# Kernel optimization log

Measured on AMD Instinct MI355X. Metric: run time of the kernel, lower is better.

## Reference

```python
import jax, jax.numpy as jnp
import numpy as np

N = 50000      # nodes
E = 800000     # edges (avg degree 16)
F_IN = 128     # num_node_features
D = 64         # embedding_size (= per-head out_channels)
H = 4          # heads
ED = 20        # edge_dim (hardcoded in module)
SLOPE = 0.2    # GATv2 leaky_relu negative slope
N_LAYERS = 3   # conv applied 3 times with shared weights


def setup_inputs() -> dict:
    key = jax.random.key(0)
    ks = jax.random.split(key, 12)
    s = 0.1
    return {
        "x": jax.random.normal(ks[0], (N, F_IN), jnp.float32),
        "edge_attr": jax.random.normal(ks[1], (E, 2), jnp.float32),
        "edge_index": jax.random.randint(ks[2], (2, E), 0, N, dtype=jnp.int32),
        # f: Linear(F_IN, D)
        "f_W": jax.random.normal(ks[3], (F_IN, D), jnp.float32) * s,
        "f_b": jnp.zeros((D,), jnp.float32),
        # fe: Linear(2, ED)
        "fe_W": jax.random.normal(ks[4], (2, ED), jnp.float32) * s,
        "fe_b": jnp.zeros((ED,), jnp.float32),
        # GATv2Conv lin_l / lin_r: Linear(D, H*D)
        "Wl": jax.random.normal(ks[5], (D, H * D), jnp.float32) * s,
        "bl": jnp.zeros((H * D,), jnp.float32),
        "Wr": jax.random.normal(ks[6], (D, H * D), jnp.float32) * s,
        "br": jnp.zeros((H * D,), jnp.float32),
        # lin_edge: Linear(ED, H*D, bias=False)
        "We": jax.random.normal(ks[7], (ED, H * D), jnp.float32) * s,
        # attention vector att: [H, D]
        "att": jax.random.normal(ks[8], (H, D), jnp.float32) * s,
        # final bias (concat=False -> size D)
        "bias": jnp.zeros((D,), jnp.float32),
    }


def _gatv2_conv(h, e_emb, src, dst, Wl, bl, Wr, br, We, att, bias):
    # h: [N, D], e_emb: [E, ED], src/dst: [E]
    xl = (h @ Wl + bl).reshape(-1, H, D)        # source transform  [N,H,D]
    xr = (h @ Wr + br).reshape(-1, H, D)        # target transform  [N,H,D]
    ee = (e_emb @ We).reshape(-1, H, D)         # edge transform    [E,H,D]
    m = jax.nn.leaky_relu(xl[src] + xr[dst] + ee, SLOPE)  # [E,H,D]
    score = jnp.einsum('ehd,hd->eh', m, att)    # [E,H]
    # segment softmax over incoming edges of each dst node
    smax = jax.ops.segment_max(score, dst, num_segments=N)   # [N,H]
    ex = jnp.exp(score - smax[dst])
    denom = jax.ops.segment_sum(ex, dst, num_segments=N)     # [N,H]
    alpha = ex / denom[dst]                                  # [E,H]
    out = jax.ops.segment_sum(alpha[:, :, None] * xl[src], dst, num_segments=N)  # [N,H,D]
    return out.mean(axis=1) + bias              # concat=False -> head mean, [N,D]


def reference(x, edge_attr, edge_index, f_W, f_b, fe_W, fe_b, Wl, bl, Wr, br, We, att, bias):
    src, dst = edge_index[0], edge_index[1]
    h = jax.nn.relu(x @ f_W + f_b)
    e = jax.nn.relu(edge_attr @ fe_W + fe_b)
    for _ in range(N_LAYERS):
        h = jax.nn.relu(_gatv2_conv(h, e, src, dst, Wl, bl, Wr, br, We, att, bias))
    return h
```

## Files before the change

kernel.cpp:

```cpp
#include <hip/hip_runtime.h>
#include <math.h>

typedef float v2f __attribute__((ext_vector_type(2)));

#define LN2_INV 1.4426950408889634f

__device__ __forceinline__ float fexp2(float x) {
#if __has_builtin(__builtin_amdgcn_exp2f)
    return __builtin_amdgcn_exp2f(x);
#else
    return exp2f(x);
#endif
}

__device__ __forceinline__ v2f pk_fma(v2f a, v2f b, v2f c) {
    asm("v_pk_fma_f32 %0, %1, %2, %0" : "+v"(c) : "v"(a), "v"(b));
    return c;
}
__device__ __forceinline__ v2f pk_fma_s(v2f a_s, v2f b, v2f c) {
    asm("v_pk_fma_f32 %0, %1, %2, %0" : "+v"(c) : "s"(a_s), "v"(b));
    return c;
}
__device__ __forceinline__ v2f pk_mul_s(v2f a_s, v2f b) {
    v2f d;
    asm("v_pk_mul_f32 %0, %1, %2" : "=v"(d) : "s"(a_s), "v"(b));
    return d;
}

#define DPP_ROW_ADD(V, CTRL) \
    V += __int_as_float(__builtin_amdgcn_update_dpp(0, __float_as_int(V), CTRL, 0xf, 0xf, true));

__global__ __launch_bounds__(256) void k_h0(const float* __restrict__ x,
                                            const float* __restrict__ fW,
                                            const float* __restrict__ fb,
                                            float* __restrict__ h0) {
    __shared__ __align__(16) float xs[8 * 128];
    int t = threadIdx.x;
    int base = blockIdx.x * 8;
#pragma unroll
    for (int r = 0; r < 4; ++r) { int j = r * 256 + t; xs[j] = x[base * 128 + j]; }
    __syncthreads();
    int c = t & 63, half = t >> 6;
    float acc0 = fb[c], acc1 = fb[c];
    int m0 = half, m1 = half + 4;
#pragma unroll 8
    for (int k0 = 0; k0 < 128; k0 += 4) {
        float4 a = *(const float4*)&xs[m0 * 128 + k0];
        float4 b = *(const float4*)&xs[m1 * 128 + k0];
        float w0 = fW[(k0 + 0) * 64 + c], w1 = fW[(k0 + 1) * 64 + c];
        float w2 = fW[(k0 + 2) * 64 + c], w3 = fW[(k0 + 3) * 64 + c];
        acc0 = fmaf(a.x, w0, fmaf(a.y, w1, fmaf(a.z, w2, fmaf(a.w, w3, acc0))));
        acc1 = fmaf(b.x, w0, fmaf(b.y, w1, fmaf(b.z, w2, fmaf(b.w, w3, acc1))));
    }
    h0[(base + m0) * 64 + c] = fmaxf(acc0, 0.f);
    h0[(base + m1) * 64 + c] = fmaxf(acc1, 0.f);
}

__global__ __launch_bounds__(256) void k_xlxr(const float* __restrict__ h,
                                              const float* __restrict__ Wl,
                                              const float* __restrict__ Wr,
                                              const float* __restrict__ bl,
                                              const float* __restrict__ br,
                                              float* __restrict__ xl,
                                              float* __restrict__ xr) {
    __shared__ __align__(16) float hs[16 * 64];
    int t = threadIdx.x;
    int base = blockIdx.x * 16;
#pragma unroll
    for (int r = 0; r < 4; ++r) hs[r * 256 + t] = h[base * 64 + r * 256 + t];
    __syncthreads();
    float bL = bl[t], bR = br[t];
    float accl[16], accr[16];
#pragma unroll
    for (int m = 0; m < 16; ++m) { accl[m] = bL; accr[m] = bR; }
#pragma unroll 4
    for (int k0 = 0; k0 < 64; k0 += 4) {
        float wl[4], wr[4];
#pragma unroll
        for (int q = 0; q < 4; ++q) {
            wl[q] = Wl[(k0 + q) * 256 + t];
            wr[q] = Wr[(k0 + q) * 256 + t];
        }
#pragma unroll
        for (int m = 0; m < 16; ++m) {
            float4 hv = *(const float4*)&hs[m * 64 + k0];
            accl[m] = fmaf(hv.x, wl[0], fmaf(hv.y, wl[1], fmaf(hv.z, wl[2], fmaf(hv.w, wl[3], accl[m]))));
            accr[m] = fmaf(hv.x, wr[0], fmaf(hv.y, wr[1], fmaf(hv.z, wr[2], fmaf(hv.w, wr[3], accr[m]))));
        }
    }
#pragma unroll
    for (int m = 0; m < 16; ++m) {
        xl[(base + m) * 256 + t] = accl[m];
        xr[(base + m) * 256 + t] = accr[m];
    }
}

__global__ void k_zero(int* __restrict__ deg, int* __restrict__ counter,
                       int* __restrict__ rec, int Nn, int Ee) {
    int i = blockIdx.x * 256 + threadIdx.x;
    if (i < Nn) deg[i] = 0;
    if (i == 0) *counter = 0;
    if (blockIdx.x == 0 && threadIdx.x < 96) rec[(size_t)Ee * 24 + threadIdx.x] = 0;
}

__global__ void k_count(const int* __restrict__ dstArr, int* __restrict__ deg, int Ee) {
    int e = blockIdx.x * 256 + threadIdx.x;
    if (e < Ee) atomicAdd(&deg[dstArr[e]], 1);
}

__global__ void k_alloc(const int* __restrict__ deg, int* __restrict__ counter,
                        int* __restrict__ start, int* __restrict__ cursor, int Nn) {
    int n = blockIdx.x * 256 + threadIdx.x;
    if (n < Nn) {
        int d = deg[n];
        int b = atomicAdd(counter, d);
        start[n] = b;
        cursor[n] = b;
    }
}

__global__ void k_fill(const int* __restrict__ dstArr, const int* __restrict__ srcArr,
                       const float* __restrict__ eattr, const float* __restrict__ feW,
                       const float* __restrict__ feb, int* __restrict__ cursor,
                       int* __restrict__ rec, int Ee) {
    int e = blockIdx.x * 256 + threadIdx.x;
    if (e >= Ee) return;
    float a0 = eattr[2 * e], a1 = eattr[2 * e + 1];
    int p = atomicAdd(&cursor[dstArr[e]], 1);
    float* r = (float*)(rec + (size_t)p * 24);
    float s[20];
#pragma unroll
    for (int k = 0; k < 20; ++k)
        s[k] = fmaxf(fmaf(a0, feW[k], fmaf(a1, feW[20 + k], feb[k])), 0.f);
#pragma unroll
    for (int j = 0; j < 5; ++j)
        ((float4*)r)[j] = make_float4(s[4 * j], s[4 * j + 1], s[4 * j + 2], s[4 * j + 3]);
    ((int*)r)[20] = srcArr[e];
}

#define LOAD_BLOCK(SK, E_) do {                                              \
    const float* _rp = rf + (size_t)(E_) * 24;                               \
    _Pragma("unroll")                                                        \
    for (int _k = 0; _k < 20; ++_k) SK[_k] = _rp[_k];                        \
} while (0)

#define COMPUTE_EDGE(SK, XL) do {                                            \
    v2f _sp0 = {SK[0], SK[1]};                                               \
    v2f _a0 = pk_mul_s(_sp0, weI0[0]);                                       \
    v2f _a1 = pk_mul_s(_sp0, weI1[0]);                                       \
    v2f _a2 = pk_mul_s(_sp0, weI2[0]);                                       \
    v2f _a3 = pk_mul_s(_sp0, weI3[0]);                                       \
    _Pragma("unroll")                                                        \
    for (int _p = 1; _p < 10; ++_p) {                                        \
        v2f _s = {SK[2 * _p], SK[2 * _p + 1]};                               \
        _a0 = pk_fma_s(_s, weI0[_p], _a0);                                   \
        _a1 = pk_fma_s(_s, weI1[_p], _a1);                                   \
        _a2 = pk_fma_s(_s, weI2[_p], _a2);                                   \
        _a3 = pk_fma_s(_s, weI3[_p], _a3);                                   \
    }                                                                        \
    float _v0 = (XL.x + xrv.x) + (_a0.x + _a0.y);                            \
    float _v1 = (XL.y + xrv.y) + (_a1.x + _a1.y);                            \
    float _v2 = (XL.z + xrv.z) + (_a2.x + _a2.y);                            \
    float _v3 = (XL.w + xrv.w) + (_a3.x + _a3.y);                            \
    float _m0 = fmaxf(_v0, 0.2f * _v0);                                      \
    float _m1 = fmaxf(_v1, 0.2f * _v1);                                      \
    float _m2 = fmaxf(_v2, 0.2f * _v2);                                      \
    float _m3 = fmaxf(_v3, 0.2f * _v3);                                      \
    float _ps = fmaf(at0, _m0, fmaf(at1, _m1, fmaf(at2, _m2, at3 * _m3)));   \
    DPP_ROW_ADD(_ps, 0x111)                                                  \
    DPP_ROW_ADD(_ps, 0x112)                                                  \
    DPP_ROW_ADD(_ps, 0x114)                                                  \
    DPP_ROW_ADD(_ps, 0x118)                                                  \
    float _sc = __int_as_float(                                              \
        __builtin_amdgcn_ds_bpermute(bperm, __float_as_int(_ps)));           \
    float _w = fexp2(_sc);                                                   \
    l += _w;                                                                 \
    v2f _w2 = {_w, _w};                                                      \
    v2f _xl01 = {XL.x, XL.y}, _xl23 = {XL.z, XL.w};                          \
    acc01 = pk_fma(_w2, _xl01, acc01);                                       \
    acc23 = pk_fma(_w2, _xl23, acc23);                                       \
} while (0)

__global__ __launch_bounds__(256, 3) void k_edge(
    const float4* __restrict__ xl4p, const float4* __restrict__ xr4p,
    const float* __restrict__ att, const float4* __restrict__ We4,
    const int* __restrict__ rec, const int* __restrict__ start,
    const int* __restrict__ deg, const float* __restrict__ bias,
    float* __restrict__ hout, int Nn) {
    const int lane = threadIdx.x & 63;
    const int n = (int)((blockIdx.x * 256u + threadIdx.x) >> 6);
    if (n >= Nn) return;

    const int dn = __builtin_amdgcn_readfirstlane(deg[n]);
    float4 bias4 = ((const float4*)bias)[lane & 15];
    if (dn == 0) {
        if (lane < 16) {
            float4 o = make_float4(fmaxf(bias4.x, 0.f), fmaxf(bias4.y, 0.f),
                                   fmaxf(bias4.z, 0.f), fmaxf(bias4.w, 0.f));
            ((float4*)hout)[(size_t)n * 16 + lane] = o;
        }
        return;
    }
    const int s0 = __builtin_amdgcn_readfirstlane(start[n]);
    const float* rf = (const float*)rec + (size_t)s0 * 24;
    const int* ri = rec + (size_t)s0 * 24;

    float4 attv = ((const float4*)att)[lane];
    float at0 = attv.x * LN2_INV, at1 = attv.y * LN2_INV;
    float at2 = attv.z * LN2_INV, at3 = attv.w * LN2_INV;
    float4 xrv = xr4p[(size_t)n * 64 + lane];
    v2f weI0[10], weI1[10], weI2[10], weI3[10];
#pragma unroll
    for (int p = 0; p < 10; ++p) {
        float4 w0 = We4[(2 * p) * 64 + lane];
        float4 w1 = We4[(2 * p + 1) * 64 + lane];
        weI0[p].x = w0.x; weI0[p].y = w1.x;
        weI1[p].x = w0.y; weI1[p].y = w1.y;
        weI2[p].x = w0.z; weI2[p].y = w1.z;
        weI3[p].x = w0.w; weI3[p].y = w1.w;
    }
    const int bperm = ((lane & 48) | 15) << 2;

    v2f acc01 = {0.f, 0.f}, acc23 = {0.f, 0.f};
    float l = 0.f;

    float skA[20], skB[20];
    LOAD_BLOCK(skA, 0);
    LOAD_BLOCK(skB, 1);
    int sA0 = ri[20];
    int sB0 = ri[44];
    float4 xlA = xl4p[(size_t)(unsigned)sA0 * 64 + lane];
    float4 xlB = xl4p[(size_t)(unsigned)sB0 * 64 + lane];
    int srcA = ri[2 * 24 + 20];
    int srcB = ri[3 * 24 + 20];

    const int nfull = dn >> 1;
    for (int t = 0; t < nfull; ++t) {
        float4 xlA2 = xl4p[(size_t)(unsigned)srcA * 64 + lane];
        srcA = ri[(size_t)(2 * t + 4) * 24 + 20];
        COMPUTE_EDGE(skA, xlA);
        LOAD_BLOCK(skA, 2 * t + 2);
        xlA = xlA2;
        float4 xlB2 = xl4p[(size_t)(unsigned)srcB * 64 + lane];
        srcB = ri[(size_t)(2 * t + 5) * 24 + 20];
        COMPUTE_EDGE(skB, xlB);
        LOAD_BLOCK(skB, 2 * t + 3);
        xlB = xlB2;
    }
    if (dn & 1) COMPUTE_EDGE(skA, xlA);

    float inv = 0.25f / l;
    float4 r = make_float4(acc01.x * inv, acc01.y * inv, acc23.x * inv, acc23.y * inv);
    r.x += __shfl_xor(r.x, 16, 64); r.x += __shfl_xor(r.x, 32, 64);
    r.y += __shfl_xor(r.y, 16, 64); r.y += __shfl_xor(r.y, 32, 64);
    r.z += __shfl_xor(r.z, 16, 64); r.z += __shfl_xor(r.z, 32, 64);
    r.w += __shfl_xor(r.w, 16, 64); r.w += __shfl_xor(r.w, 32, 64);
    if (lane < 16) {
        float4 o = make_float4(fmaxf(r.x + bias4.x, 0.f), fmaxf(r.y + bias4.y, 0.f),
                               fmaxf(r.z + bias4.z, 0.f), fmaxf(r.w + bias4.w, 0.f));
        ((float4*)hout)[(size_t)n * 16 + lane] = o;
    }
}

extern "C" void kernel_launch(void* const* d_in, const int* in_sizes, int n_in,
                              void* d_out, int out_size, void* d_ws, size_t ws_size,
                              hipStream_t stream) {
    const float* x     = (const float*)d_in[0];
    const float* eattr = (const float*)d_in[1];
    const int*   eidx  = (const int*)d_in[2];
    const float* fW    = (const float*)d_in[3];
    const float* fb    = (const float*)d_in[4];
    const float* feW   = (const float*)d_in[5];
    const float* feb   = (const float*)d_in[6];
    const float* Wl    = (const float*)d_in[7];
    const float* bl    = (const float*)d_in[8];
    const float* Wr    = (const float*)d_in[9];
    const float* br    = (const float*)d_in[10];
    const float* We    = (const float*)d_in[11];
    const float* att   = (const float*)d_in[12];
    const float* bias  = (const float*)d_in[13];
    float* out = (float*)d_out;

    const int N = in_sizes[0] / 128;
    const int E = in_sizes[1] / 2;
    const int* srcArr = eidx;
    const int* dstArr = eidx + E;

    char* p = (char*)d_ws;
    auto alloc = [&](size_t bytes) -> char* {
        char* r = p;
        p += (bytes + 255) & ~(size_t)255;
        return r;
    };
    float* hA   = (float*)alloc((size_t)N * 64 * 4);
    float* hB   = (float*)alloc((size_t)N * 64 * 4);
    float* xl   = (float*)alloc((size_t)N * 256 * 4);
    float* xr   = (float*)alloc((size_t)N * 256 * 4);
    int* deg    = (int*)alloc((size_t)N * 4);
    int* start  = (int*)alloc((size_t)N * 4);
    int* cursor = (int*)alloc((size_t)N * 4);
    int* counter = (int*)alloc(256);
    int* rec    = (int*)alloc((size_t)(E + 4) * 24 * 4);

    k_h0<<<N / 8, 256, 0, stream>>>(x, fW, fb, hA);
    k_zero<<<(N + 255) / 256, 256, 0, stream>>>(deg, counter, rec, N, E);
    k_count<<<(E + 255) / 256, 256, 0, stream>>>(dstArr, deg, E);
    k_alloc<<<(N + 255) / 256, 256, 0, stream>>>(deg, counter, start, cursor, N);
    k_fill<<<(E + 255) / 256, 256, 0, stream>>>(dstArr, srcArr, eattr, feW, feb,
                                                cursor, rec, E);

    const float* hin = hA;
    for (int layer = 0; layer < 3; ++layer) {
        float* hout = (layer == 2) ? out : ((layer == 0) ? hB : hA);
        k_xlxr<<<N / 16, 256, 0, stream>>>(hin, Wl, Wr, bl, br, xl, xr);
        k_edge<<<(N * 64) / 256, 256, 0, stream>>>(
            (const float4*)xl, (const float4*)xr, att, (const float4*)We,
            rec, start, deg, bias, hout, N);
        hin = hout;
    }
}
```

Measured before the change: 967.2 us.

## Split edge source indices into separate array and deepen xl gather prefetch

```diff
diff --git a/kernel.cpp b/kernel.cpp
--- a/kernel.cpp
+++ b/kernel.cpp
@@ -2,6 +2,7 @@
 #include <math.h>
 
 typedef float v2f __attribute__((ext_vector_type(2)));
+typedef float v4f __attribute__((ext_vector_type(4)));
 
 #define LN2_INV 1.4426950408889634f
 
@@ -26,6 +27,9 @@
     asm("v_pk_mul_f32 %0, %1, %2" : "=v"(d) : "s"(a_s), "v"(b));
     return d;
 }
+
+#define PIN_V(X) asm("" : "+v"(X))
+#define PIN_S(X) asm("" : "+s"(X))
 
 #define DPP_ROW_ADD(V, CTRL) \
     V += __int_as_float(__builtin_amdgcn_update_dpp(0, __float_as_int(V), CTRL, 0xf, 0xf, true));
@@ -96,11 +100,13 @@
 }
 
 __global__ void k_zero(int* __restrict__ deg, int* __restrict__ counter,
-                       int* __restrict__ rec, int Nn, int Ee) {
+                       int* __restrict__ rec, int* __restrict__ sidx,
+                       int Nn, int Ee) {
     int i = blockIdx.x * 256 + threadIdx.x;
     if (i < Nn) deg[i] = 0;
     if (i == 0) *counter = 0;
-    if (blockIdx.x == 0 && threadIdx.x < 96) rec[(size_t)Ee * 24 + threadIdx.x] = 0;
+    if (blockIdx.x == 0 && threadIdx.x < 160) rec[(size_t)Ee * 20 + threadIdx.x] = 0;
+    if (blockIdx.x == 0 && threadIdx.x < 8) sidx[Ee + threadIdx.x] = 0;
 }
 
 __global__ void k_count(const int* __restrict__ dstArr, int* __restrict__ deg, int Ee) {
@@ -122,12 +128,12 @@
 __global__ void k_fill(const int* __restrict__ dstArr, const int* __restrict__ srcArr,
                        const float* __restrict__ eattr, const float* __restrict__ feW,
                        const float* __restrict__ feb, int* __restrict__ cursor,
-                       int* __restrict__ rec, int Ee) {
+                       int* __restrict__ rec, int* __restrict__ sidx, int Ee) {
     int e = blockIdx.x * 256 + threadIdx.x;
     if (e >= Ee) return;
     float a0 = eattr[2 * e], a1 = eattr[2 * e + 1];
     int p = atomicAdd(&cursor[dstArr[e]], 1);
-    float* r = (float*)(rec + (size_t)p * 24);
+    float* r = (float*)(rec + (size_t)p * 20);
     float s[20];
 #pragma unroll
     for (int k = 0; k < 20; ++k)
@@ -135,11 +141,11 @@
 #pragma unroll
     for (int j = 0; j < 5; ++j)
         ((float4*)r)[j] = make_float4(s[4 * j], s[4 * j + 1], s[4 * j + 2], s[4 * j + 3]);
-    ((int*)r)[20] = srcArr[e];
+    sidx[p] = srcArr[e];
 }
 
 #define LOAD_BLOCK(SK, E_) do {                                              \
-    const float* _rp = rf + (size_t)(E_) * 24;                               \
+    const float* _rp = rf + (size_t)(E_) * 20;                               \
     _Pragma("unroll")                                                        \
     for (int _k = 0; _k < 20; ++_k) SK[_k] = _rp[_k];                        \
 } while (0)
@@ -182,33 +188,33 @@
 } while (0)
 
 __global__ __launch_bounds__(256, 3) void k_edge(
-    const float4* __restrict__ xl4p, const float4* __restrict__ xr4p,
+    const v4f* __restrict__ xl4p, const v4f* __restrict__ xr4p,
     const float* __restrict__ att, const float4* __restrict__ We4,
-    const int* __restrict__ rec, const int* __restrict__ start,
-    const int* __restrict__ deg, const float* __restrict__ bias,
-    float* __restrict__ hout, int Nn) {
+    const int* __restrict__ rec, const int* __restrict__ sidx,
+    const int* __restrict__ start, const int* __restrict__ deg,
+    const float* __restrict__ bias, float* __restrict__ hout, int Nn) {
     const int lane = threadIdx.x & 63;
     const int n = (int)((blockIdx.x * 256u + threadIdx.x) >> 6);
     if (n >= Nn) return;
 
     const int dn = __builtin_amdgcn_readfirstlane(deg[n]);
-    float4 bias4 = ((const float4*)bias)[lane & 15];
+    v4f bias4 = ((const v4f*)bias)[lane & 15];
     if (dn == 0) {
         if (lane < 16) {
-            float4 o = make_float4(fmaxf(bias4.x, 0.f), fmaxf(bias4.y, 0.f),
-                                   fmaxf(bias4.z, 0.f), fmaxf(bias4.w, 0.f));
-            ((float4*)hout)[(size_t)n * 16 + lane] = o;
+            v4f o = {fmaxf(bias4.x, 0.f), fmaxf(bias4.y, 0.f),
+                     fmaxf(bias4.z, 0.f), fmaxf(bias4.w, 0.f)};
+            ((v4f*)hout)[(size_t)n * 16 + lane] = o;
         }
         return;
     }
     const int s0 = __builtin_amdgcn_readfirstlane(start[n]);
-    const float* rf = (const float*)rec + (size_t)s0 * 24;
-    const int* ri = rec + (size_t)s0 * 24;
+    const float* rf = (const float*)rec + (size_t)s0 * 20;
+    const int* sI = sidx + s0;
 
     float4 attv = ((const float4*)att)[lane];
     float at0 = attv.x * LN2_INV, at1 = attv.y * LN2_INV;
     float at2 = attv.z * LN2_INV, at3 = attv.w * LN2_INV;
-    float4 xrv = xr4p[(size_t)n * 64 + lane];
+    v4f xrv = xr4p[(size_t)n * 64 + lane];
     v2f weI0[10], weI1[10], weI2[10], weI3[10];
 #pragma unroll
     for (int p = 0; p < 10; ++p) {
@@ -227,38 +233,43 @@
     float skA[20], skB[20];
     LOAD_BLOCK(skA, 0);
     LOAD_BLOCK(skB, 1);
-    int sA0 = ri[20];
-    int sB0 = ri[44];
-    float4 xlA = xl4p[(size_t)(unsigned)sA0 * 64 + lane];
-    float4 xlB = xl4p[(size_t)(unsigned)sB0 * 64 + lane];
-    int srcA = ri[2 * 24 + 20];
-    int srcB = ri[3 * 24 + 20];
+    int e0 = sI[0], e1 = sI[1], e2 = sI[2], e3 = sI[3];
+    int srcA = sI[4], srcB = sI[5];
+    v4f xlA  = xl4p[(size_t)(unsigned)e0 * 64 + lane];
+    v4f xlB  = xl4p[(size_t)(unsigned)e1 * 64 + lane];
+    v4f xlA1 = xl4p[(size_t)(unsigned)e2 * 64 + lane];
+    v4f xlB1 = xl4p[(size_t)(unsigned)e3 * 64 + lane];
 
     const int nfull = dn >> 1;
+#pragma unroll 2
     for (int t = 0; t < nfull; ++t) {
-        float4 xlA2 = xl4p[(size_t)(unsigned)srcA * 64 + lane];
-        srcA = ri[(size_t)(2 * t + 4) * 24 + 20];
+        v4f xlA2 = xl4p[(size_t)(unsigned)srcA * 64 + lane];
+        PIN_V(xlA2);
+        srcA = sI[2 * t + 6];
+        PIN_S(srcA);
         COMPUTE_EDGE(skA, xlA);
         LOAD_BLOCK(skA, 2 * t + 2);
-        xlA = xlA2;
-        float4 xlB2 = xl4p[(size_t)(unsigned)srcB * 64 + lane];
-        srcB = ri[(size_t)(2 * t + 5) * 24 + 20];
+        xlA = xlA1; xlA1 = xlA2;
+        v4f xlB2 = xl4p[(size_t)(unsigned)srcB * 64 + lane];
+        PIN_V(xlB2);
+        srcB = sI[2 * t + 7];
+        PIN_S(srcB);
         COMPUTE_EDGE(skB, xlB);
         LOAD_BLOCK(skB, 2 * t + 3);
-        xlB = xlB2;
+        xlB = xlB1; xlB1 = xlB2;
     }
     if (dn & 1) COMPUTE_EDGE(skA, xlA);
 
     float inv = 0.25f / l;
-    float4 r = make_float4(acc01.x * inv, acc01.y * inv, acc23.x * inv, acc23.y * inv);
+    v4f r = {acc01.x * inv, acc01.y * inv, acc23.x * inv, acc23.y * inv};
     r.x += __shfl_xor(r.x, 16, 64); r.x += __shfl_xor(r.x, 32, 64);
     r.y += __shfl_xor(r.y, 16, 64); r.y += __shfl_xor(r.y, 32, 64);
     r.z += __shfl_xor(r.z, 16, 64); r.z += __shfl_xor(r.z, 32, 64);
     r.w += __shfl_xor(r.w, 16, 64); r.w += __shfl_xor(r.w, 32, 64);
     if (lane < 16) {
-        float4 o = make_float4(fmaxf(r.x + bias4.x, 0.f), fmaxf(r.y + bias4.y, 0.f),
-                               fmaxf(r.z + bias4.z, 0.f), fmaxf(r.w + bias4.w, 0.f));
-        ((float4*)hout)[(size_t)n * 16 + lane] = o;
+        v4f o = {fmaxf(r.x + bias4.x, 0.f), fmaxf(r.y + bias4.y, 0.f),
+                 fmaxf(r.z + bias4.z, 0.f), fmaxf(r.w + bias4.w, 0.f)};
+        ((v4f*)hout)[(size_t)n * 16 + lane] = o;
     }
 }
 
@@ -300,22 +311,23 @@
     int* start  = (int*)alloc((size_t)N * 4);
     int* cursor = (int*)alloc((size_t)N * 4);
     int* counter = (int*)alloc(256);
-    int* rec    = (int*)alloc((size_t)(E + 4) * 24 * 4);
+    int* rec    = (int*)alloc((size_t)(E + 8) * 20 * 4);
+    int* sidx   = (int*)alloc((size_t)(E + 8) * 4);
 
     k_h0<<<N / 8, 256, 0, stream>>>(x, fW, fb, hA);
-    k_zero<<<(N + 255) / 256, 256, 0, stream>>>(deg, counter, rec, N, E);
+    k_zero<<<(N + 255) / 256, 256, 0, stream>>>(deg, counter, rec, sidx, N, E);
     k_count<<<(E + 255) / 256, 256, 0, stream>>>(dstArr, deg, E);
     k_alloc<<<(N + 255) / 256, 256, 0, stream>>>(deg, counter, start, cursor, N);
     k_fill<<<(E + 255) / 256, 256, 0, stream>>>(dstArr, srcArr, eattr, feW, feb,
-                                                cursor, rec, E);
+                                                cursor, rec, sidx, E);
 
     const float* hin = hA;
     for (int layer = 0; layer < 3; ++layer) {
         float* hout = (layer == 2) ? out : ((layer == 0) ? hB : hA);
         k_xlxr<<<N / 16, 256, 0, stream>>>(hin, Wl, Wr, bl, br, xl, xr);
         k_edge<<<(N * 64) / 256, 256, 0, stream>>>(
-            (const float4*)xl, (const float4*)xr, att, (const float4*)We,
-            rec, start, deg, bias, hout, N);
+            (const v4f*)xl, (const v4f*)xr, att, (const float4*)We,
+            rec, sidx, start, deg, bias, hout, N);
         hin = hout;
     }
 }
```

Measured after the change: 953.6 us. Within noise of the previous version (-1.4%).

## Prefetch edge sources via readlane, deepen xl prefetch, vectorize record loads

Applied to the files above, without the earlier changes.

```diff
diff --git a/kernel.cpp b/kernel.cpp
--- a/kernel.cpp
+++ b/kernel.cpp
@@ -13,21 +13,21 @@
 #endif
 }
 
+__device__ __forceinline__ int rdlane_i(int v, int k) {
+    return __builtin_amdgcn_readlane(v, k);
+}
+
 __device__ __forceinline__ v2f pk_fma(v2f a, v2f b, v2f c) {
     asm("v_pk_fma_f32 %0, %1, %2, %0" : "+v"(c) : "v"(a), "v"(b));
     return c;
 }
-__device__ __forceinline__ v2f pk_fma_s(v2f a_s, v2f b, v2f c) {
-    asm("v_pk_fma_f32 %0, %1, %2, %0" : "+v"(c) : "s"(a_s), "v"(b));
-    return c;
-}
-__device__ __forceinline__ v2f pk_mul_s(v2f a_s, v2f b) {
+__device__ __forceinline__ v2f pk_mul(v2f a, v2f b) {
     v2f d;
-    asm("v_pk_mul_f32 %0, %1, %2" : "=v"(d) : "s"(a_s), "v"(b));
+    asm("v_pk_mul_f32 %0, %1, %2" : "=v"(d) : "v"(a), "v"(b));
     return d;
 }
 
-#define DPP_ROW_ADD(V, CTRL) \
+#define DPP_ADD(V, CTRL) \
     V += __int_as_float(__builtin_amdgcn_update_dpp(0, __float_as_int(V), CTRL, 0xf, 0xf, true));
 
 __global__ __launch_bounds__(256) void k_h0(const float* __restrict__ x,
@@ -138,25 +138,30 @@
     ((int*)r)[20] = srcArr[e];
 }
 
-#define LOAD_BLOCK(SK, E_) do {                                              \
-    const float* _rp = rf + (size_t)(E_) * 24;                               \
-    _Pragma("unroll")                                                        \
-    for (int _k = 0; _k < 20; ++_k) SK[_k] = _rp[_k];                        \
+#define VLOAD_REC(SK4, E_) do {                                              \
+    const float4* _rp = (const float4*)(rf + (size_t)(E_) * 24);             \
+    SK4[0] = _rp[0]; SK4[1] = _rp[1]; SK4[2] = _rp[2];                       \
+    SK4[3] = _rp[3]; SK4[4] = _rp[4];                                        \
 } while (0)
 
-#define COMPUTE_EDGE(SK, XL) do {                                            \
-    v2f _sp0 = {SK[0], SK[1]};                                               \
-    v2f _a0 = pk_mul_s(_sp0, weI0[0]);                                       \
-    v2f _a1 = pk_mul_s(_sp0, weI1[0]);                                       \
-    v2f _a2 = pk_mul_s(_sp0, weI2[0]);                                       \
-    v2f _a3 = pk_mul_s(_sp0, weI3[0]);                                       \
+#define COMPUTE_EDGE(SK4, XL) do {                                           \
+    v2f _a0, _a1, _a2, _a3;                                                  \
+    {                                                                        \
+        v2f _sp = {SK4[0].x, SK4[0].y};                                      \
+        _a0 = pk_mul(_sp, weI0[0]);                                          \
+        _a1 = pk_mul(_sp, weI1[0]);                                          \
+        _a2 = pk_mul(_sp, weI2[0]);                                          \
+        _a3 = pk_mul(_sp, weI3[0]);                                          \
+    }                                                                        \
     _Pragma("unroll")                                                        \
     for (int _p = 1; _p < 10; ++_p) {                                        \
-        v2f _s = {SK[2 * _p], SK[2 * _p + 1]};                               \
-        _a0 = pk_fma_s(_s, weI0[_p], _a0);                                   \
-        _a1 = pk_fma_s(_s, weI1[_p], _a1);                                   \
-        _a2 = pk_fma_s(_s, weI2[_p], _a2);                                   \
-        _a3 = pk_fma_s(_s, weI3[_p], _a3);                                   \
+        int _j = _p >> 1;                                                    \
+        v2f _sp = (_p & 1) ? (v2f){SK4[_j].z, SK4[_j].w}                     \
+                           : (v2f){SK4[_j].x, SK4[_j].y};                    \
+        _a0 = pk_fma(_sp, weI0[_p], _a0);                                    \
+        _a1 = pk_fma(_sp, weI1[_p], _a1);                                    \
+        _a2 = pk_fma(_sp, weI2[_p], _a2);                                    \
+        _a3 = pk_fma(_sp, weI3[_p], _a3);                                    \
     }                                                                        \
     float _v0 = (XL.x + xrv.x) + (_a0.x + _a0.y);                            \
     float _v1 = (XL.y + xrv.y) + (_a1.x + _a1.y);                            \
@@ -167,13 +172,11 @@
     float _m2 = fmaxf(_v2, 0.2f * _v2);                                      \
     float _m3 = fmaxf(_v3, 0.2f * _v3);                                      \
     float _ps = fmaf(at0, _m0, fmaf(at1, _m1, fmaf(at2, _m2, at3 * _m3)));   \
-    DPP_ROW_ADD(_ps, 0x111)                                                  \
-    DPP_ROW_ADD(_ps, 0x112)                                                  \
-    DPP_ROW_ADD(_ps, 0x114)                                                  \
-    DPP_ROW_ADD(_ps, 0x118)                                                  \
-    float _sc = __int_as_float(                                              \
-        __builtin_amdgcn_ds_bpermute(bperm, __float_as_int(_ps)));           \
-    float _w = fexp2(_sc);                                                   \
+    DPP_ADD(_ps, 0x121)                                                      \
+    DPP_ADD(_ps, 0x122)                                                      \
+    DPP_ADD(_ps, 0x124)                                                      \
+    DPP_ADD(_ps, 0x128)                                                      \
+    float _w = fexp2(_ps);                                                   \
     l += _w;                                                                 \
     v2f _w2 = {_w, _w};                                                      \
     v2f _xl01 = {XL.x, XL.y}, _xl23 = {XL.z, XL.w};                          \
@@ -192,11 +195,11 @@
     if (n >= Nn) return;
 
     const int dn = __builtin_amdgcn_readfirstlane(deg[n]);
-    float4 bias4 = ((const float4*)bias)[lane & 15];
     if (dn == 0) {
         if (lane < 16) {
-            float4 o = make_float4(fmaxf(bias4.x, 0.f), fmaxf(bias4.y, 0.f),
-                                   fmaxf(bias4.z, 0.f), fmaxf(bias4.w, 0.f));
+            float4 b4 = ((const float4*)bias)[lane];
+            float4 o = make_float4(fmaxf(b4.x, 0.f), fmaxf(b4.y, 0.f),
+                                   fmaxf(b4.z, 0.f), fmaxf(b4.w, 0.f));
             ((float4*)hout)[(size_t)n * 16 + lane] = o;
         }
         return;
@@ -204,6 +207,9 @@
     const int s0 = __builtin_amdgcn_readfirstlane(start[n]);
     const float* rf = (const float*)rec + (size_t)s0 * 24;
     const int* ri = rec + (size_t)s0 * 24;
+
+    const int lc = (lane < dn) ? lane : (dn - 1);
+    int srcv = rec[(size_t)(s0 + lc) * 24 + 20];
 
     float4 attv = ((const float4*)att)[lane];
     float at0 = attv.x * LN2_INV, at1 = attv.y * LN2_INV;
@@ -219,35 +225,40 @@
         weI2[p].x = w0.z; weI2[p].y = w1.z;
         weI3[p].x = w0.w; weI3[p].y = w1.w;
     }
-    const int bperm = ((lane & 48) | 15) << 2;
 
     v2f acc01 = {0.f, 0.f}, acc23 = {0.f, 0.f};
     float l = 0.f;
 
-    float skA[20], skB[20];
-    LOAD_BLOCK(skA, 0);
-    LOAD_BLOCK(skB, 1);
-    int sA0 = ri[20];
-    int sB0 = ri[44];
-    float4 xlA = xl4p[(size_t)(unsigned)sA0 * 64 + lane];
-    float4 xlB = xl4p[(size_t)(unsigned)sB0 * 64 + lane];
-    int srcA = ri[2 * 24 + 20];
-    int srcB = ri[3 * 24 + 20];
+    auto get_src = [&](int j) -> int {
+        return (j < 64) ? rdlane_i(srcv, j) : ri[(size_t)j * 24 + 20];
+    };
+
+    float4 skA4[5], skB4[5];
+    VLOAD_REC(skA4, 0);
+    VLOAD_REC(skB4, 1);
+    int j1 = (1 < dn) ? 1 : (dn - 1);
+    int j2 = (2 < dn) ? 2 : (dn - 1);
+    int j3 = (3 < dn) ? 3 : (dn - 1);
+    float4 xlA  = xl4p[(size_t)(unsigned)get_src(0) * 64 + lane];
+    float4 xlB  = xl4p[(size_t)(unsigned)get_src(j1) * 64 + lane];
+    float4 xlA1 = xl4p[(size_t)(unsigned)get_src(j2) * 64 + lane];
+    float4 xlB1 = xl4p[(size_t)(unsigned)get_src(j3) * 64 + lane];
 
     const int nfull = dn >> 1;
     for (int t = 0; t < nfull; ++t) {
-        float4 xlA2 = xl4p[(size_t)(unsigned)srcA * 64 + lane];
-        srcA = ri[(size_t)(2 * t + 4) * 24 + 20];
-        COMPUTE_EDGE(skA, xlA);
-        LOAD_BLOCK(skA, 2 * t + 2);
-        xlA = xlA2;
-        float4 xlB2 = xl4p[(size_t)(unsigned)srcB * 64 + lane];
-        srcB = ri[(size_t)(2 * t + 5) * 24 + 20];
-        COMPUTE_EDGE(skB, xlB);
-        LOAD_BLOCK(skB, 2 * t + 3);
-        xlB = xlB2;
-    }
-    if (dn & 1) COMPUTE_EDGE(skA, xlA);
+        int i = 2 * t;
+        int jA = (i + 4 < dn) ? (i + 4) : (dn - 1);
+        int jB = (i + 5 < dn) ? (i + 5) : (dn - 1);
+        float4 xlA2 = xl4p[(size_t)(unsigned)get_src(jA) * 64 + lane];
+        float4 xlB2 = xl4p[(size_t)(unsigned)get_src(jB) * 64 + lane];
+        COMPUTE_EDGE(skA4, xlA);
+        VLOAD_REC(skA4, i + 2);
+        COMPUTE_EDGE(skB4, xlB);
+        VLOAD_REC(skB4, i + 3);
+        xlA = xlA1; xlA1 = xlA2;
+        xlB = xlB1; xlB1 = xlB2;
+    }
+    if (dn & 1) COMPUTE_EDGE(skA4, xlA);
 
     float inv = 0.25f / l;
     float4 r = make_float4(acc01.x * inv, acc01.y * inv, acc23.x * inv, acc23.y * inv);
@@ -256,8 +267,9 @@
     r.z += __shfl_xor(r.z, 16, 64); r.z += __shfl_xor(r.z, 32, 64);
     r.w += __shfl_xor(r.w, 16, 64); r.w += __shfl_xor(r.w, 32, 64);
     if (lane < 16) {
-        float4 o = make_float4(fmaxf(r.x + bias4.x, 0.f), fmaxf(r.y + bias4.y, 0.f),
-                               fmaxf(r.z + bias4.z, 0.f), fmaxf(r.w + bias4.w, 0.f));
+        float4 b4 = ((const float4*)bias)[lane];
+        float4 o = make_float4(fmaxf(r.x + b4.x, 0.f), fmaxf(r.y + b4.y, 0.f),
+                               fmaxf(r.z + b4.z, 0.f), fmaxf(r.w + b4.w, 0.f));
         ((float4*)hout)[(size_t)n * 16 + lane] = o;
     }
 }
```

Result: slower. 1.293 ms (+33.7%).
